# Kernel tuning notes

Measured on AMD Instinct MI355X. Metric: run time of the kernel, lower is better.

The kernel has to match this reference:

```python
import jax, jax.numpy as jnp
import numpy as np

N, DIM, K = 8192, 64, 32
ALPHA = 1.0

def setup_inputs() -> dict:
    key = jax.random.key(0)
    k1, k2, k3, k4, k5, k6 = jax.random.split(key, 6)
    s = 1.0 / np.sqrt(DIM)
    return {
        "node_emb": jax.random.normal(k1, (N, DIM), dtype=jnp.float32),
        "noise": jax.random.uniform(k2, (N, N), dtype=jnp.float32),
        "W1": jax.random.uniform(k3, (DIM, DIM), minval=-s, maxval=s, dtype=jnp.float32),
        "b1": jax.random.uniform(k4, (DIM,), minval=-s, maxval=s, dtype=jnp.float32),
        "W2": jax.random.uniform(k5, (DIM, DIM), minval=-s, maxval=s, dtype=jnp.float32),
        "b2": jax.random.uniform(k6, (DIM,), minval=-s, maxval=s, dtype=jnp.float32),
    }

def reference(node_emb, noise, W1, b1, W2, b2):
    # dual Linear + exact (erf) GELU, matching torch F.gelu default
    v1 = jax.nn.gelu(ALPHA * (node_emb @ W1.T + b1), approximate=False)  # [N, dim]
    v2 = jax.nn.gelu(ALPHA * (node_emb @ W2.T + b2), approximate=False)  # [N, dim]
    # asymmetric adjacency: relu(v1 v2^T - v2 v1^T)  -> [N, N]
    adj = jax.nn.relu(v1 @ v2.T - v2 @ v1.T)
    # top-k per row on noise-perturbed scores (tie-break), scatter 1s into mask
    _, idx = jax.lax.top_k(adj + noise * 0.01, K)            # idx: [N, K]
    mask = jnp.zeros((N, N), dtype=adj.dtype).at[jnp.arange(N)[:, None], idx].set(1.0)
    return adj * mask
```

## Files before the change

### kernel.cpp

```cpp
#include <hip/hip_runtime.h>
#include <math.h>


__global__ __launch_bounds__(256) void compute_vv(
    const float* __restrict__ emb, const float* __restrict__ W1,
    const float* __restrict__ b1, const float* __restrict__ W2,
    const float* __restrict__ b2, float* __restrict__ VV)
{
    __shared__ float sW[2][64 * 65];
    __shared__ float sb[2][64];
    __shared__ float semb[2][64];
    int tid = threadIdx.x;
    for (int t = tid; t < 64 * 64; t += 256) {
        int o = t >> 6, k = t & 63;
        sW[0][o * 65 + k] = W1[t];
        sW[1][o * 65 + k] = W2[t];
    }
    if (tid < 64) { sb[0][tid] = b1[tid]; sb[1][tid] = b2[tid]; }
    int i0 = blockIdx.x * 2;
    if (tid < 128) semb[tid >> 6][tid & 63] = emb[(size_t)i0 * 64 + tid];
    __syncthreads();

    int li = tid >> 7;
    int c  = tid & 127;
    int o  = c >> 1;
    int w  = c & 1;
    const float* wr = &sW[w][o * 65];
    const float* e  = &semb[li][0];
    float acc = 0.0f;
#pragma unroll
    for (int k = 0; k < 64; ++k) acc = fmaf(e[k], wr[k], acc);
    float x = acc + sb[w][o];
    double xd = (double)x;
    double g = 0.5 * xd * (1.0 + erf(xd * 0.70710678118654752440));
    VV[(size_t)(i0 + li) * 128 + c] = (float)g;
}

__global__ __launch_bounds__(256, 2) void adj_gemm_tri(
    const float* __restrict__ VV, float* __restrict__ out)
{
    int bi = blockIdx.x, bj = blockIdx.y;
    if (bj < bi) return;

    __shared__ __align__(16) float smem[16896];
    float* Ar1 = smem;
    float* Ar2 = smem + 4224;
    float* Ac1 = smem + 8448;
    float* Ac2 = smem + 12672;

    int tid  = threadIdx.x;
    int trow = tid >> 4, tcol = tid & 15;
    const int grow = bi * 128, gcol = bj * 128;

    float d1[8][8], d2[8][8];
#pragma unroll
    for (int r = 0; r < 8; ++r)
#pragma unroll
        for (int c = 0; c < 8; ++c) { d1[r][c] = 0.0f; d2[r][c] = 0.0f; }

    const float4* VV4 = (const float4*)VV;
    for (int kb = 0; kb < 2; ++kb) {
        __syncthreads();
        for (int g = tid; g < 2048; g += 256) {
            int row = g >> 4, off = g & 15;
            float4 f = VV4[(size_t)(grow + row) * 32 + kb * 16 + off];
            float4 h = VV4[(size_t)(gcol + row) * 32 + kb * 16 + off];
            int kk = off * 2;
            Ar1[kk * 132 + row] = f.x; Ar2[kk * 132 + row] = f.y;
            Ar1[(kk + 1) * 132 + row] = f.z; Ar2[(kk + 1) * 132 + row] = f.w;
            Ac1[kk * 132 + row] = h.x; Ac2[kk * 132 + row] = h.y;
            Ac1[(kk + 1) * 132 + row] = h.z; Ac2[(kk + 1) * 132 + row] = h.w;
        }
        __syncthreads();
#pragma unroll 2
        for (int k = 0; k < 32; ++k) {
            float rv1[8], rv2[8], cv1[8], cv2[8];
            *(float4*)&rv1[0] = *(const float4*)&Ar1[k * 132 + trow * 4];
            *(float4*)&rv1[4] = *(const float4*)&Ar1[k * 132 + 64 + trow * 4];
            *(float4*)&rv2[0] = *(const float4*)&Ar2[k * 132 + trow * 4];
            *(float4*)&rv2[4] = *(const float4*)&Ar2[k * 132 + 64 + trow * 4];
            *(float4*)&cv1[0] = *(const float4*)&Ac1[k * 132 + tcol * 4];
            *(float4*)&cv1[4] = *(const float4*)&Ac1[k * 132 + 64 + tcol * 4];
            *(float4*)&cv2[0] = *(const float4*)&Ac2[k * 132 + tcol * 4];
            *(float4*)&cv2[4] = *(const float4*)&Ac2[k * 132 + 64 + tcol * 4];
#pragma unroll
            for (int r = 0; r < 8; ++r)
#pragma unroll
                for (int c = 0; c < 8; ++c) {
                    d1[r][c] = fmaf(rv1[r], cv2[c], d1[r][c]);
                    d2[r][c] = fmaf(rv2[r], cv1[c], d2[r][c]);
                }
        }
    }

#pragma unroll
    for (int rr = 0; rr < 8; ++rr) {
        int r = (rr < 4) ? (trow * 4 + rr) : (64 + trow * 4 + (rr - 4));
        float4 o0, o1;
        o0.x = fmaxf(d1[rr][0] - d2[rr][0], 0.0f);
        o0.y = fmaxf(d1[rr][1] - d2[rr][1], 0.0f);
        o0.z = fmaxf(d1[rr][2] - d2[rr][2], 0.0f);
        o0.w = fmaxf(d1[rr][3] - d2[rr][3], 0.0f);
        o1.x = fmaxf(d1[rr][4] - d2[rr][4], 0.0f);
        o1.y = fmaxf(d1[rr][5] - d2[rr][5], 0.0f);
        o1.z = fmaxf(d1[rr][6] - d2[rr][6], 0.0f);
        o1.w = fmaxf(d1[rr][7] - d2[rr][7], 0.0f);
        float* op = out + (size_t)(grow + r) * 8192 + gcol;
        *(float4*)(op + tcol * 4)      = o0;
        *(float4*)(op + 64 + tcol * 4) = o1;
    }

    __syncthreads();
    float (*tT)[132] = (float(*)[132])smem;
#pragma unroll
    for (int rr = 0; rr < 8; ++rr) {
        int r = (rr < 4) ? (trow * 4 + rr) : (64 + trow * 4 + (rr - 4));
#pragma unroll
        for (int cc = 0; cc < 8; ++cc) {
            int c = (cc < 4) ? (tcol * 4 + cc) : (64 + tcol * 4 + (cc - 4));
            tT[c][r] = fmaxf(d2[rr][cc] - d1[rr][cc], 0.0f);
        }
    }
    __syncthreads();
    for (int g = tid; g < 4096; g += 256) {
        int orow_ = g >> 5, off = g & 31;
        float4 v = *(const float4*)&tT[orow_][off * 4];
        *(float4*)(out + (size_t)(gcol + orow_) * 8192 + grow + off * 4) = v;
    }
}

__device__ __forceinline__ unsigned fkey(float f) {
    unsigned u = __float_as_uint(f);
    return (u & 0x80000000u) ? ~u : (u | 0x80000000u);
}

__device__ __forceinline__ void select_bin1024(
    const unsigned* __restrict__ hist, unsigned* __restrict__ chs,
    int tid, int krem, int* __restrict__ sh_bin, int* __restrict__ sh_above)
{
    chs[tid] = hist[tid * 4 + 0] + hist[tid * 4 + 1] +
               hist[tid * 4 + 2] + hist[tid * 4 + 3];
    __syncthreads();
    if (tid < 64) {
        unsigned g = chs[tid * 4 + 0] + chs[tid * 4 + 1] +
                     chs[tid * 4 + 2] + chs[tid * 4 + 3];
        unsigned v = g;
#pragma unroll
        for (int off = 1; off < 64; off <<= 1) {
            unsigned o = __shfl_down(v, off);
            if (tid + off < 64) v += o;
        }
        unsigned above = v - g;
        if (above < (unsigned)krem && (unsigned)krem <= above + g) {
            unsigned cum = above;
            int bin = -1;
            for (int c = 3; c >= 0 && bin < 0; --c) {
                unsigned cs = chs[tid * 4 + c];
                if (cum + cs >= (unsigned)krem) {
                    int cb = tid * 4 + c;
                    for (int b = 3; b >= 0; --b) {
                        unsigned h = hist[cb * 4 + b];
                        if (cum + h >= (unsigned)krem) { bin = cb * 4 + b; break; }
                        cum += h;
                    }
                } else cum += cs;
            }
            *sh_bin = bin; *sh_above = (int)cum;
        }
    }
    __syncthreads();
}

#define TK_CAP 1024

__global__ __launch_bounds__(256) void topk_select(
    const float* __restrict__ noise, float* __restrict__ out)
{
    __shared__ unsigned hist[1024];
    __shared__ unsigned chs[256];
    __shared__ unsigned ckey[TK_CAP];
    __shared__ int      cidx[TK_CAP];
    __shared__ int      wlist[32];
    __shared__ float    wval[32];
    __shared__ int      sh_bin, sh_above;
    __shared__ unsigned sh_cnt;

    int tid = threadIdx.x;
    int row = blockIdx.x;
    float*       orow = out   + (size_t)row * 8192;
    const float* nrow = noise + (size_t)row * 8192;
    const float4* o4 = (const float4*)orow;
    const float4* n4 = (const float4*)nrow;

    for (int i = tid; i < 1024; i += 256) hist[i] = 0u;
    __syncthreads();

    unsigned kk[32];
#pragma unroll
    for (int i = 0; i < 8; ++i) {
        int t = tid + i * 256;
        float4 a  = o4[t];
        float4 nz = n4[t];
        unsigned q0 = fkey(__fadd_rn(a.x, __fmul_rn(nz.x, 0.01f)));
        unsigned q1 = fkey(__fadd_rn(a.y, __fmul_rn(nz.y, 0.01f)));
        unsigned q2 = fkey(__fadd_rn(a.z, __fmul_rn(nz.z, 0.01f)));
        unsigned q3 = fkey(__fadd_rn(a.w, __fmul_rn(nz.w, 0.01f)));
        kk[i * 4 + 0] = q0; kk[i * 4 + 1] = q1;
        kk[i * 4 + 2] = q2; kk[i * 4 + 3] = q3;
        atomicAdd(&hist[q0 >> 22], 1u);
        atomicAdd(&hist[q1 >> 22], 1u);
        atomicAdd(&hist[q2 >> 22], 1u);
        atomicAdd(&hist[q3 >> 22], 1u);
    }
    __syncthreads();

    int shiftv = 22;
    select_bin1024(hist, chs, tid, 32, &sh_bin, &sh_above);
    unsigned Tf = ((unsigned)sh_bin) << 22;
    int cum = sh_above;

    int cnt;
    for (;;) {
        if (tid == 0) sh_cnt = 0u;
        __syncthreads();
#pragma unroll
        for (int i = 0; i < 32; ++i) {
            if (kk[i] >= Tf) {
                unsigned p = atomicAdd(&sh_cnt, 1u);
                if (p < TK_CAP) {
                    ckey[p] = kk[i];
                    cidx[p] = tid * 4 + (i >> 2) * 1024 + (i & 3);
                }
            }
        }
        __syncthreads();
        cnt = (int)sh_cnt;
        if (cnt <= TK_CAP || shiftv <= 2) break;
        int prevShift = shiftv;
        unsigned prevTop = Tf >> prevShift;
        shiftv -= 10;
        for (int i = tid; i < 1024; i += 256) hist[i] = 0u;
        __syncthreads();
#pragma unroll
        for (int i = 0; i < 32; ++i) {
            unsigned k = kk[i];
            if ((k >> prevShift) == prevTop)
                atomicAdd(&hist[(k >> shiftv) & 0x3FFu], 1u);
        }
        __syncthreads();
        select_bin1024(hist, chs, tid, 32 - cum, &sh_bin, &sh_above);
        Tf |= ((unsigned)sh_bin) << shiftv;
        cum += sh_above;
    }
    if (cnt > TK_CAP) cnt = TK_CAP;

    for (int t = tid; t < cnt; t += 256) {
        unsigned mk = ckey[t];
        int mi = cidx[t];
        int rank = 0;
        for (int j = 0; j < cnt; ++j) {
            unsigned ok = ckey[j];
            rank += (ok > mk || (ok == mk && cidx[j] < mi)) ? 1 : 0;
        }
        if (rank < 32) wlist[rank] = mi;
    }
    __syncthreads();
    if (tid < 32) wval[tid] = orow[wlist[tid]];
    __syncthreads();
    float4 z = make_float4(0.0f, 0.0f, 0.0f, 0.0f);
#pragma unroll
    for (int i = 0; i < 8; ++i) ((float4*)orow)[tid + i * 256] = z;
    __syncthreads();
    if (tid < 32) orow[wlist[tid]] = wval[tid];
}

extern "C" void kernel_launch(void* const* d_in, const int* in_sizes, int n_in,
                              void* d_out, int out_size, void* d_ws, size_t ws_size,
                              hipStream_t stream) {
    (void)in_sizes; (void)n_in; (void)out_size; (void)ws_size;
    const float* emb   = (const float*)d_in[0];
    const float* noise = (const float*)d_in[1];
    const float* W1    = (const float*)d_in[2];
    const float* b1    = (const float*)d_in[3];
    const float* W2    = (const float*)d_in[4];
    const float* b2    = (const float*)d_in[5];
    float* out = (float*)d_out;
    float* VV  = (float*)d_ws;

    hipLaunchKernelGGL(compute_vv, dim3(4096), dim3(256), 0, stream,
                       emb, W1, b1, W2, b2, VV);
    hipLaunchKernelGGL(adj_gemm_tri, dim3(64, 64), dim3(256), 0, stream, VV, out);
    hipLaunchKernelGGL(topk_select, dim3(8192), dim3(256), 0, stream, noise, out);
}
```

Measured before the change: 673.4 us.

## Replace radix-key top-k with linear value-binned histogram selection and bitmask writeback

The top-k kernel now bins the perturbed scores by linear value ranges instead of by the high bits of an order-preserving integer key. It assumes scores are nonnegative and mostly tiny, using a coarse pass over values above a skip threshold and a fine fallback pass below it, so the first pass should isolate far fewer candidates. The final write keeps adj values in registers and uses a shared bitmask to emit a masked row in one pass, replacing the separate zeroing pass followed by a scatter. The scheme depends on the value distribution, since adj is at least zero and noise*0.01 lies in [0,0.01), and refinement is capped at a few passes, which could truncate candidates if many values tie closely.

Result: faster. 656.8 us (-2.5%).

```diff
diff --git a/kernel.cpp b/kernel.cpp
--- a/kernel.cpp
+++ b/kernel.cpp
@@ -129,14 +129,21 @@
     }
 }
 
-__device__ __forceinline__ unsigned fkey(float f) {
-    unsigned u = __float_as_uint(f);
-    return (u & 0x80000000u) ? ~u : (u | 0x80000000u);
+#define SKIPV 0.015625f
+#define CAP   1024
+
+__device__ __forceinline__ int binof(float s, float lo, float scale, float inv) {
+    int b = (int)((s - lo) * scale);
+    if (b > 1023) b = 1023;
+    if (lo + (float)b * inv > s) --b;
+    else if (b < 1023 && lo + (float)(b + 1) * inv <= s) ++b;
+    return b;
 }
 
 __device__ __forceinline__ void select_bin1024(
     const unsigned* __restrict__ hist, unsigned* __restrict__ chs,
-    int tid, int krem, int* __restrict__ sh_bin, int* __restrict__ sh_above)
+    int tid, int krem, int* __restrict__ sh_bin, int* __restrict__ sh_above,
+    unsigned* __restrict__ sh_total)
 {
     chs[tid] = hist[tid * 4 + 0] + hist[tid * 4 + 1] +
                hist[tid * 4 + 2] + hist[tid * 4 + 3];
@@ -150,6 +157,7 @@
             unsigned o = __shfl_down(v, off);
             if (tid + off < 64) v += o;
         }
+        if (tid == 0) *sh_total = v;
         unsigned above = v - g;
         if (above < (unsigned)krem && (unsigned)krem <= above + g) {
             unsigned cum = above;
@@ -171,19 +179,16 @@
     __syncthreads();
 }
 
-#define TK_CAP 1024
-
-__global__ __launch_bounds__(256) void topk_select(
+__global__ __launch_bounds__(256) void topk_linear(
     const float* __restrict__ noise, float* __restrict__ out)
 {
     __shared__ unsigned hist[1024];
     __shared__ unsigned chs[256];
-    __shared__ unsigned ckey[TK_CAP];
-    __shared__ int      cidx[TK_CAP];
-    __shared__ int      wlist[32];
-    __shared__ float    wval[32];
+    __shared__ float    cs[CAP];
+    __shared__ int      ci[CAP];
+    __shared__ unsigned flags[256];
     __shared__ int      sh_bin, sh_above;
-    __shared__ unsigned sh_cnt;
+    __shared__ unsigned sh_total, sh_cnt;
 
     int tid = threadIdx.x;
     int row = blockIdx.x;
@@ -192,86 +197,109 @@
     const float4* o4 = (const float4*)orow;
     const float4* n4 = (const float4*)nrow;
 
+    float ss[32], aa[32];
+#pragma unroll
+    for (int i = 0; i < 8; ++i) {
+        float4 a  = o4[tid + i * 256];
+        float4 nz = n4[tid + i * 256];
+        aa[i * 4 + 0] = a.x; ss[i * 4 + 0] = __fadd_rn(a.x, __fmul_rn(nz.x, 0.01f));
+        aa[i * 4 + 1] = a.y; ss[i * 4 + 1] = __fadd_rn(a.y, __fmul_rn(nz.y, 0.01f));
+        aa[i * 4 + 2] = a.z; ss[i * 4 + 2] = __fadd_rn(a.z, __fmul_rn(nz.z, 0.01f));
+        aa[i * 4 + 3] = a.w; ss[i * 4 + 3] = __fadd_rn(a.w, __fmul_rn(nz.w, 0.01f));
+    }
     for (int i = tid; i < 1024; i += 256) hist[i] = 0u;
-    __syncthreads();
-
-    unsigned kk[32];
-#pragma unroll
-    for (int i = 0; i < 8; ++i) {
-        int t = tid + i * 256;
-        float4 a  = o4[t];
-        float4 nz = n4[t];
-        unsigned q0 = fkey(__fadd_rn(a.x, __fmul_rn(nz.x, 0.01f)));
-        unsigned q1 = fkey(__fadd_rn(a.y, __fmul_rn(nz.y, 0.01f)));
-        unsigned q2 = fkey(__fadd_rn(a.z, __fmul_rn(nz.z, 0.01f)));
-        unsigned q3 = fkey(__fadd_rn(a.w, __fmul_rn(nz.w, 0.01f)));
-        kk[i * 4 + 0] = q0; kk[i * 4 + 1] = q1;
-        kk[i * 4 + 2] = q2; kk[i * 4 + 3] = q3;
-        atomicAdd(&hist[q0 >> 22], 1u);
-        atomicAdd(&hist[q1 >> 22], 1u);
-        atomicAdd(&hist[q2 >> 22], 1u);
-        atomicAdd(&hist[q3 >> 22], 1u);
-    }
-    __syncthreads();
-
-    int shiftv = 22;
-    select_bin1024(hist, chs, tid, 32, &sh_bin, &sh_above);
-    unsigned Tf = ((unsigned)sh_bin) << 22;
-    int cum = sh_above;
+    flags[tid] = 0u;
+    __syncthreads();
+
+#pragma unroll
+    for (int s = 0; s < 32; ++s) {
+        if (ss[s] >= SKIPV)
+            atomicAdd(&hist[binof(ss[s], 0.0f, 128.0f, 0.0078125f)], 1u);
+    }
+    __syncthreads();
+
+    select_bin1024(hist, chs, tid, 32, &sh_bin, &sh_above, &sh_total);
+    float Tf, lo, width;
+    int krem;
+    if (sh_total >= 32u) {
+        Tf    = (float)sh_bin * 0.0078125f;
+        krem  = 32 - sh_above;
+        lo    = Tf; width = 0.0078125f;
+    } else {
+        int kr2 = 32 - (int)sh_total;
+        __syncthreads();
+        for (int i = tid; i < 1024; i += 256) hist[i] = 0u;
+        __syncthreads();
+#pragma unroll
+        for (int s = 0; s < 32; ++s) {
+            if (ss[s] < SKIPV)
+                atomicAdd(&hist[binof(ss[s], 0.0f, 65536.0f, 1.525878906e-5f)], 1u);
+        }
+        __syncthreads();
+        select_bin1024(hist, chs, tid, kr2, &sh_bin, &sh_above, &sh_total);
+        Tf    = (float)sh_bin * 1.525878906e-5f;
+        krem  = kr2 - sh_above;
+        lo    = Tf; width = 1.525878906e-5f;
+    }
 
     int cnt;
-    for (;;) {
+    for (int pass = 0;; ++pass) {
         if (tid == 0) sh_cnt = 0u;
         __syncthreads();
 #pragma unroll
-        for (int i = 0; i < 32; ++i) {
-            if (kk[i] >= Tf) {
+        for (int s = 0; s < 32; ++s) {
+            if (ss[s] >= Tf) {
                 unsigned p = atomicAdd(&sh_cnt, 1u);
-                if (p < TK_CAP) {
-                    ckey[p] = kk[i];
-                    cidx[p] = tid * 4 + (i >> 2) * 1024 + (i & 3);
+                if (p < CAP) {
+                    cs[p] = ss[s];
+                    ci[p] = tid * 4 + (s >> 2) * 1024 + (s & 3);
                 }
             }
         }
         __syncthreads();
         cnt = (int)sh_cnt;
-        if (cnt <= TK_CAP || shiftv <= 2) break;
-        int prevShift = shiftv;
-        unsigned prevTop = Tf >> prevShift;
-        shiftv -= 10;
+        if (cnt <= CAP || pass >= 2) break;
         for (int i = tid; i < 1024; i += 256) hist[i] = 0u;
         __syncthreads();
-#pragma unroll
-        for (int i = 0; i < 32; ++i) {
-            unsigned k = kk[i];
-            if ((k >> prevShift) == prevTop)
-                atomicAdd(&hist[(k >> shiftv) & 0x3FFu], 1u);
-        }
-        __syncthreads();
-        select_bin1024(hist, chs, tid, 32 - cum, &sh_bin, &sh_above);
-        Tf |= ((unsigned)sh_bin) << shiftv;
-        cum += sh_above;
-    }
-    if (cnt > TK_CAP) cnt = TK_CAP;
+        float scale = 1024.0f / width;
+        float inv   = width * 0.0009765625f;
+#pragma unroll
+        for (int s = 0; s < 32; ++s) {
+            if (ss[s] >= lo && ss[s] < lo + width)
+                atomicAdd(&hist[binof(ss[s], lo, scale, inv)], 1u);
+        }
+        __syncthreads();
+        select_bin1024(hist, chs, tid, krem, &sh_bin, &sh_above, &sh_total);
+        Tf    = lo + (float)sh_bin * inv;
+        krem -= sh_above;
+        lo    = Tf; width = inv;
+    }
+    if (cnt > CAP) cnt = CAP;
 
     for (int t = tid; t < cnt; t += 256) {
-        unsigned mk = ckey[t];
-        int mi = cidx[t];
+        float msv = cs[t];
+        int   mi  = ci[t];
         int rank = 0;
         for (int j = 0; j < cnt; ++j) {
-            unsigned ok = ckey[j];
-            rank += (ok > mk || (ok == mk && cidx[j] < mi)) ? 1 : 0;
-        }
-        if (rank < 32) wlist[rank] = mi;
-    }
-    __syncthreads();
-    if (tid < 32) wval[tid] = orow[wlist[tid]];
-    __syncthreads();
-    float4 z = make_float4(0.0f, 0.0f, 0.0f, 0.0f);
-#pragma unroll
-    for (int i = 0; i < 8; ++i) ((float4*)orow)[tid + i * 256] = z;
-    __syncthreads();
-    if (tid < 32) orow[wlist[tid]] = wval[tid];
+            float os = cs[j];
+            rank += (os > msv || (os == msv && ci[j] < mi)) ? 1 : 0;
+        }
+        if (rank < 32) atomicOr(&flags[mi >> 5], 1u << (mi & 31));
+    }
+    __syncthreads();
+
+#pragma unroll
+    for (int i = 0; i < 8; ++i) {
+        int j0 = 4 * (tid + i * 256);
+        unsigned w = flags[j0 >> 5];
+        int sh = j0 & 31;
+        float4 o;
+        o.x = ((w >> (sh + 0)) & 1u) ? aa[i * 4 + 0] : 0.0f;
+        o.y = ((w >> (sh + 1)) & 1u) ? aa[i * 4 + 1] : 0.0f;
+        o.z = ((w >> (sh + 2)) & 1u) ? aa[i * 4 + 2] : 0.0f;
+        o.w = ((w >> (sh + 3)) & 1u) ? aa[i * 4 + 3] : 0.0f;
+        ((float4*)orow)[tid + i * 256] = o;
+    }
 }
 
 extern "C" void kernel_launch(void* const* d_in, const int* in_sizes, int n_in,
@@ -290,5 +318,5 @@
     hipLaunchKernelGGL(compute_vv, dim3(4096), dim3(256), 0, stream,
                        emb, W1, b1, W2, b2, VV);
     hipLaunchKernelGGL(adj_gemm_tri, dim3(64, 64), dim3(256), 0, stream, VV, out);
-    hipLaunchKernelGGL(topk_select, dim3(8192), dim3(256), 0, stream, noise, out);
-}
+    hipLaunchKernelGGL(topk_linear, dim3(8192), dim3(256), 0, stream, noise, out);
+}
```
